# Kernel tuning notes

Hardware: AMD Instinct MI355X
Metric: run time of the kernel (lower is better)

The kernel has to match this reference:

```python
import jax, jax.numpy as jnp
import numpy as np

N, M, D = 8192, 8192, 1024

def setup_inputs() -> dict:
    key = jax.random.key(0)
    k1, k2 = jax.random.split(key)
    encoder_outputs = jax.random.normal(k1, (N, D), dtype=jnp.float32)
    fact_emb = jax.random.normal(k2, (M, D), dtype=jnp.float32)
    return {"encoder_outputs": encoder_outputs, "fact_emb": fact_emb}

def reference(encoder_outputs, fact_emb):
    # energy: [N, M] = encoder_outputs @ fact_emb^T (unscaled)
    energy = jnp.einsum('nd,md->nm', encoder_outputs, fact_emb)
    weights = jax.nn.softmax(energy, axis=1)          # softmax over facts
    outputs = jnp.einsum('nm,md->nd', weights, fact_emb)
    return (outputs, weights)
```

## Files before the change

kernel.cpp:

```cpp
#include <hip/hip_runtime.h>
#include <hip/hip_bf16.h>
#include <math.h>
#include <stdint.h>

#define N_ROWS 8192
#define M_FACTS 8192
#define D_DIM 1024

typedef __bf16 bf16x8_t __attribute__((ext_vector_type(8)));
typedef __bf16 bf16x4_t __attribute__((ext_vector_type(4)));
typedef float f32x4_t __attribute__((ext_vector_type(4)));

#define BM 128
#define BN 128
#define BK 32
#define PADK 40

__device__ __forceinline__ void gload_lds16(const void* g, void* lds) {
  __builtin_amdgcn_global_load_lds(
      (__attribute__((address_space(1))) void*)(uintptr_t)g,
      (__attribute__((address_space(3))) void*)(uint32_t)(uintptr_t)lds,
      16, 0, 0);
}


__global__ __launch_bounds__(256) void split_hi_lo(const float* __restrict__ X,
                                                   __bf16* __restrict__ H,
                                                   __bf16* __restrict__ L) {
  int i = blockIdx.x * 256 + threadIdx.x;
  float4 v = ((const float4*)X)[i];
  float f[4] = {v.x, v.y, v.z, v.w};
  bf16x4_t h, l;
#pragma unroll
  for (int q = 0; q < 4; q++) {
    __bf16 hh = (__bf16)f[q];
    h[q] = hh;
    l[q] = (__bf16)(f[q] - (float)hh);
  }
  ((bf16x4_t*)H)[i] = h;
  ((bf16x4_t*)L)[i] = l;
}

__global__ __launch_bounds__(256) void split_concat_E(const float* __restrict__ X,
                                                      __bf16* __restrict__ A2) {
  int idx = blockIdx.x * 256 + threadIdx.x;
  int n = idx >> 8, d4 = idx & 255;
  float4 v = ((const float4*)X)[idx];
  float f[4] = {v.x, v.y, v.z, v.w};
  bf16x4_t h, l;
#pragma unroll
  for (int q = 0; q < 4; q++) {
    __bf16 hh = (__bf16)f[q];
    h[q] = hh;
    l[q] = (__bf16)(f[q] - (float)hh);
  }
  size_t base = (size_t)n * 3072 + d4 * 4;
  *(bf16x4_t*)(A2 + base) = h;
  *(bf16x4_t*)(A2 + base + 1024) = l;
  *(bf16x4_t*)(A2 + base + 2048) = h;
}

__global__ __launch_bounds__(256) void split_concat_F(const float* __restrict__ X,
                                                      __bf16* __restrict__ B2) {
  int idx = blockIdx.x * 256 + threadIdx.x;
  int m = idx >> 8, d4 = idx & 255;
  float4 v = ((const float4*)X)[idx];
  float f[4] = {v.x, v.y, v.z, v.w};
  bf16x4_t h, l;
#pragma unroll
  for (int q = 0; q < 4; q++) {
    __bf16 hh = (__bf16)f[q];
    h[q] = hh;
    l[q] = (__bf16)(f[q] - (float)hh);
  }
  size_t base = (size_t)m * 3072 + d4 * 4;
  *(bf16x4_t*)(B2 + base) = h;
  *(bf16x4_t*)(B2 + base + 1024) = h;
  *(bf16x4_t*)(B2 + base + 2048) = l;
}

__global__ __launch_bounds__(256) void transpose_f_bf16(const float* __restrict__ F,
                                                        __bf16* __restrict__ Ft) {
  __shared__ float t[64 * 69];
  const int tid = threadIdx.x;
  const int m0 = blockIdx.x * 64, d0 = blockIdx.y * 64;
#pragma unroll
  for (int p = 0; p < 4; p++) {
    int flat = p * 256 + tid;
    int m = flat >> 4, dq = flat & 15;
    float4 v = *(const float4*)(F + (size_t)(m0 + m) * D_DIM + d0 + dq * 4);
    t[(dq * 4 + 0) * 69 + m] = v.x;
    t[(dq * 4 + 1) * 69 + m] = v.y;
    t[(dq * 4 + 2) * 69 + m] = v.z;
    t[(dq * 4 + 3) * 69 + m] = v.w;
  }
  __syncthreads();
#pragma unroll
  for (int q = 0; q < 2; q++) {
    int id = q * 256 + tid;
    int d = id >> 3, c = id & 7;
    const float* row = t + d * 69 + c * 8;
    bf16x8_t o;
#pragma unroll
    for (int i = 0; i < 8; i++) o[i] = (__bf16)row[i];
    *(bf16x8_t*)(Ft + (size_t)(d0 + d) * M_FACTS + m0 + c * 8) = o;
  }
}

__global__ __launch_bounds__(512, 2) void gemm_ring(const __bf16* __restrict__ A,
                                                    const __bf16* __restrict__ B,
                                                    float* __restrict__ C,
                                                    int K, int lda, int ldb, int ldc) {
  __shared__ __align__(16) __bf16 sA[3][256 * 64];
  __shared__ __align__(16) __bf16 sB[3][128 * 64];
  const int tid = threadIdx.x;
  const int wave = tid >> 6, lane = tid & 63;
  const int wm = wave >> 2;
  const int wn = wave & 3;
  const int lrow = lane & 15, quad = lane >> 4;
  const int row0 = blockIdx.x * 256;
  const int col0 = blockIdx.y * 128;

  auto STAGE = [&](int slot, int kt) {
    const int ko = kt * 64;
#pragma unroll
    for (int k = 0; k < 4; k++) {
      int g = tid + 512 * k;
      int sr = g >> 3;
      int so = ((g & 7) ^ (sr & 7)) << 3;
      gload_lds16(A + (size_t)(row0 + sr) * lda + ko + so, &sA[slot][g * 8]);
    }
#pragma unroll
    for (int k = 0; k < 2; k++) {
      int g = tid + 512 * k;
      int sr = g >> 3;
      int so = ((g & 7) ^ (sr & 7)) << 3;
      gload_lds16(B + (size_t)(col0 + sr) * ldb + ko + so, &sB[slot][g * 8]);
    }
  };

  f32x4_t acc[8][2];
#pragma unroll
  for (int i = 0; i < 8; i++)
#pragma unroll
    for (int j = 0; j < 2; j++) acc[i][j] = (f32x4_t){0.f, 0.f, 0.f, 0.f};

  const int nkt = K >> 6;

  STAGE(0, 0);
  STAGE(1, 1);
  asm volatile("s_waitcnt vmcnt(6)" ::: "memory");
  __builtin_amdgcn_s_barrier();
  __builtin_amdgcn_sched_barrier(0);

  int slot = 0;
  for (int t = 0; t < nkt; ++t) {
    const __bf16* lA = &sA[slot][0];
    const __bf16* lB = &sB[slot][0];
    const int slot2 = (slot == 0) ? 2 : slot - 1;

#pragma unroll
    for (int p = 0; p < 2; ++p) {
      bf16x8_t af[4][2], bfr[2][2];
#pragma unroll
      for (int rf = 0; rf < 4; ++rf) {
        const int r = wm * 128 + p * 64 + rf * 16 + lrow;
#pragma unroll
        for (int ks = 0; ks < 2; ++ks)
          af[rf][ks] = *(const bf16x8_t*)(lA + r * 64 + (((ks * 4 + quad) ^ (r & 7)) << 3));
      }
#pragma unroll
      for (int cf = 0; cf < 2; ++cf) {
        const int c = wn * 32 + cf * 16 + lrow;
#pragma unroll
        for (int ks = 0; ks < 2; ++ks)
          bfr[cf][ks] = *(const bf16x8_t*)(lB + c * 64 + (((ks * 4 + quad) ^ (c & 7)) << 3));
      }
      if (p == 0 && t + 2 < nkt) STAGE(slot2, t + 2);
      __builtin_amdgcn_s_setprio(1);
#pragma unroll
      for (int rf = 0; rf < 4; ++rf)
#pragma unroll
        for (int cf = 0; cf < 2; ++cf)
#pragma unroll
          for (int ks = 0; ks < 2; ++ks)
            acc[p * 4 + rf][cf] = __builtin_amdgcn_mfma_f32_16x16x32_bf16(
                af[rf][ks], bfr[cf][ks], acc[p * 4 + rf][cf], 0, 0, 0);
      __builtin_amdgcn_s_setprio(0);
      if (p == 0) {
        __builtin_amdgcn_sched_barrier(0);
        __builtin_amdgcn_s_barrier();
        __builtin_amdgcn_sched_barrier(0);
      }
    }
    __builtin_amdgcn_sched_barrier(0);
    if (t + 1 < nkt) {
      if (t + 2 < nkt)
        asm volatile("s_waitcnt vmcnt(6)" ::: "memory");
      else
        asm volatile("s_waitcnt vmcnt(0)" ::: "memory");
      __builtin_amdgcn_s_barrier();
      __builtin_amdgcn_sched_barrier(0);
    }
    slot = (slot == 2) ? 0 : slot + 1;
  }

#pragma unroll
  for (int i = 0; i < 8; ++i) {
    const int rbase = row0 + wm * 128 + (i >> 2) * 64 + (i & 3) * 16 + quad * 4;
#pragma unroll
    for (int j = 0; j < 2; ++j) {
      const int c = col0 + wn * 32 + j * 16 + lrow;
#pragma unroll
      for (int r = 0; r < 4; ++r) C[(size_t)(rbase + r) * ldc + c] = acc[i][j][r];
    }
  }
}

__global__ __launch_bounds__(256) void gemm1_fast(const __bf16* __restrict__ Eh,
                                                  const __bf16* __restrict__ El,
                                                  const __bf16* __restrict__ Fh,
                                                  const __bf16* __restrict__ Fl,
                                                  float* __restrict__ C,
                                                  int row_base) {
  __shared__ __bf16 sAh[BM * BK], sAl[BM * BK], sBh[BN * BK], sBl[BN * BK];
  const int tid = threadIdx.x;
  const int wave = tid >> 6, lane = tid & 63;
  const int row0 = row_base + blockIdx.x * BM, col0 = blockIdx.y * BN;
  const int wm = wave >> 1, wn = wave & 1;
  const int lrow = lane & 15, quad = lane >> 4;

  f32x4_t acc[4][4];
#pragma unroll
  for (int i = 0; i < 4; i++)
#pragma unroll
    for (int j = 0; j < 4; j++) acc[i][j] = (f32x4_t){0.f, 0.f, 0.f, 0.f};

  for (int k0 = 0; k0 < D_DIM; k0 += BK) {
#pragma unroll
    for (int r = 0; r < 2; r++) {
      int c = (r * 4 + wave) * 64 + lane;
      int row = c >> 2;
      int ko = (c & 3) << 3;
      size_t ga = (size_t)(row0 + row) * D_DIM + k0 + ko;
      size_t gb = (size_t)(col0 + row) * D_DIM + k0 + ko;
      gload_lds16(Eh + ga, sAh + c * 8);
      gload_lds16(El + ga, sAl + c * 8);
      gload_lds16(Fh + gb, sBh + c * 8);
      gload_lds16(Fl + gb, sBl + c * 8);
    }
    __syncthreads();

    bf16x8_t ah[4], al[4], bh[4], bl[4];
#pragma unroll
    for (int i = 0; i < 4; i++) {
      int ra = (wm * 64 + i * 16 + lrow) * BK + quad * 8;
      ah[i] = *(const bf16x8_t*)(sAh + ra);
      al[i] = *(const bf16x8_t*)(sAl + ra);
      int rb = (wn * 64 + i * 16 + lrow) * BK + quad * 8;
      bh[i] = *(const bf16x8_t*)(sBh + rb);
      bl[i] = *(const bf16x8_t*)(sBl + rb);
    }
#pragma unroll
    for (int i = 0; i < 4; i++)
#pragma unroll
      for (int j = 0; j < 4; j++) {
        acc[i][j] = __builtin_amdgcn_mfma_f32_16x16x32_bf16(ah[i], bh[j], acc[i][j], 0, 0, 0);
        acc[i][j] = __builtin_amdgcn_mfma_f32_16x16x32_bf16(ah[i], bl[j], acc[i][j], 0, 0, 0);
        acc[i][j] = __builtin_amdgcn_mfma_f32_16x16x32_bf16(al[i], bh[j], acc[i][j], 0, 0, 0);
      }
    __syncthreads();
  }

#pragma unroll
  for (int i = 0; i < 4; i++) {
    int rbase = row0 + wm * 64 + i * 16 + quad * 4;
#pragma unroll
    for (int j = 0; j < 4; j++) {
      int c = col0 + wn * 64 + j * 16 + lrow;
#pragma unroll
      for (int r = 0; r < 4; r++) C[(size_t)(rbase + r) * M_FACTS + c] = acc[i][j][r];
    }
  }
}

__global__ __launch_bounds__(256) void gemm2_reg(const __bf16* __restrict__ Wb,
                                                 const __bf16* __restrict__ Ft,
                                                 float* __restrict__ O,
                                                 int out_row0) {
  __shared__ __bf16 sW[2][BM * BK];
  __shared__ __bf16 sF[2][BN * BK];
  const int tid = threadIdx.x;
  const int wave = tid >> 6, lane = tid & 63;
  const int row0 = blockIdx.x * BM;
  const int col0 = blockIdx.y * BN;
  const int wm = wave >> 1, wn = wave & 1;
  const int lrow = lane & 15, quad = lane >> 4;

  const int id0 = wave * 64 + lane;
  const int r0 = id0 >> 2, c0 = (id0 & 3) << 3;
  const int id1 = id0 + 256;
  const int r1 = id1 >> 2, c1 = (id1 & 3) << 3;

  const __bf16* gW = Wb + (size_t)row0 * M_FACTS;
  const __bf16* gF = Ft + (size_t)col0 * M_FACTS;

  f32x4_t acc[4][4];
#pragma unroll
  for (int i = 0; i < 4; i++)
#pragma unroll
    for (int j = 0; j < 4; j++) acc[i][j] = (f32x4_t){0.f, 0.f, 0.f, 0.f};

  bf16x8_t rW0, rW1, rF0, rF1;
  rW0 = *(const bf16x8_t*)(gW + (size_t)r0 * M_FACTS + c0);
  rW1 = *(const bf16x8_t*)(gW + (size_t)r1 * M_FACTS + c1);
  rF0 = *(const bf16x8_t*)(gF + (size_t)r0 * M_FACTS + c0);
  rF1 = *(const bf16x8_t*)(gF + (size_t)r1 * M_FACTS + c1);
  *(bf16x8_t*)(&sW[0][id0 * 8]) = rW0;
  *(bf16x8_t*)(&sW[0][id1 * 8]) = rW1;
  *(bf16x8_t*)(&sF[0][id0 * 8]) = rF0;
  *(bf16x8_t*)(&sF[0][id1 * 8]) = rF1;
  rW0 = *(const bf16x8_t*)(gW + (size_t)r0 * M_FACTS + BK + c0);
  rW1 = *(const bf16x8_t*)(gW + (size_t)r1 * M_FACTS + BK + c1);
  rF0 = *(const bf16x8_t*)(gF + (size_t)r0 * M_FACTS + BK + c0);
  rF1 = *(const bf16x8_t*)(gF + (size_t)r1 * M_FACTS + BK + c1);
  __syncthreads();

  const int NT = M_FACTS / BK;
  for (int it = 0; it < NT; it++) {
    const int cur = it & 1;
    bf16x8_t a[4], b[4];
#pragma unroll
    for (int i = 0; i < 4; i++) {
      a[i] = *(const bf16x8_t*)(&sW[cur][(wm * 64 + i * 16 + lrow) * BK + quad * 8]);
      b[i] = *(const bf16x8_t*)(&sF[cur][(wn * 64 + i * 16 + lrow) * BK + quad * 8]);
    }
#pragma unroll
    for (int i = 0; i < 4; i++)
#pragma unroll
      for (int j = 0; j < 4; j++)
        acc[i][j] = __builtin_amdgcn_mfma_f32_16x16x32_bf16(a[i], b[j], acc[i][j], 0, 0, 0);

    __syncthreads();
    if (it + 1 < NT) {
      const int nxt = cur ^ 1;
      *(bf16x8_t*)(&sW[nxt][id0 * 8]) = rW0;
      *(bf16x8_t*)(&sW[nxt][id1 * 8]) = rW1;
      *(bf16x8_t*)(&sF[nxt][id0 * 8]) = rF0;
      *(bf16x8_t*)(&sF[nxt][id1 * 8]) = rF1;
      if (it + 2 < NT) {
        const int ko = (it + 2) * BK;
        rW0 = *(const bf16x8_t*)(gW + (size_t)r0 * M_FACTS + ko + c0);
        rW1 = *(const bf16x8_t*)(gW + (size_t)r1 * M_FACTS + ko + c1);
        rF0 = *(const bf16x8_t*)(gF + (size_t)r0 * M_FACTS + ko + c0);
        rF1 = *(const bf16x8_t*)(gF + (size_t)r1 * M_FACTS + ko + c1);
      }
      __syncthreads();
    }
  }

#pragma unroll
  for (int i = 0; i < 4; i++) {
    int rbase = out_row0 + row0 + wm * 64 + i * 16 + quad * 4;
#pragma unroll
    for (int j = 0; j < 4; j++) {
      int c = col0 + wn * 64 + j * 16 + lrow;
#pragma unroll
      for (int r = 0; r < 4; r++) O[(size_t)(rbase + r) * D_DIM + c] = acc[i][j][r];
    }
  }
}

__global__ __launch_bounds__(256) void gemm2_mid(const float* __restrict__ W,
                                                 const __bf16* __restrict__ Ft,
                                                 float* __restrict__ O) {
  __shared__ __bf16 sW[BM * BK], sF[BN * BK];
  const int tid = threadIdx.x;
  const int wave = tid >> 6, lane = tid & 63;
  const int row0 = blockIdx.x * BM, col0 = blockIdx.y * BN;
  const int wm = wave >> 1, wn = wave & 1;
  const int lrow = lane & 15, quad = lane >> 4;

  f32x4_t acc[4][4];
#pragma unroll
  for (int i = 0; i < 4; i++)
#pragma unroll
    for (int j = 0; j < 4; j++) acc[i][j] = (f32x4_t){0.f, 0.f, 0.f, 0.f};

  for (int k0 = 0; k0 < M_FACTS; k0 += BK) {
#pragma unroll
    for (int r = 0; r < 2; r++) {
      int c = (r * 4 + wave) * 64 + lane;
      int row = c >> 2;
      int ko = (c & 3) << 3;
      gload_lds16(Ft + (size_t)(col0 + row) * M_FACTS + k0 + ko, sF + c * 8);
    }
#pragma unroll
    for (int it = 0; it < 4; it++) {
      int flat = it * 256 + tid;
      int r = flat >> 3, q = flat & 7;
      float4 v = *(const float4*)(W + (size_t)(row0 + r) * M_FACTS + k0 + q * 4);
      bf16x4_t h;
      h[0] = (__bf16)v.x;
      h[1] = (__bf16)v.y;
      h[2] = (__bf16)v.z;
      h[3] = (__bf16)v.w;
      *(bf16x4_t*)(sW + r * BK + q * 4) = h;
    }
    __syncthreads();

    bf16x8_t a[4], b[4];
#pragma unroll
    for (int i = 0; i < 4; i++) {
      a[i] = *(const bf16x8_t*)(sW + (wm * 64 + i * 16 + lrow) * BK + quad * 8);
      b[i] = *(const bf16x8_t*)(sF + (wn * 64 + i * 16 + lrow) * BK + quad * 8);
    }
#pragma unroll
    for (int i = 0; i < 4; i++)
#pragma unroll
      for (int j = 0; j < 4; j++)
        acc[i][j] = __builtin_amdgcn_mfma_f32_16x16x32_bf16(a[i], b[j], acc[i][j], 0, 0, 0);
    __syncthreads();
  }

#pragma unroll
  for (int i = 0; i < 4; i++) {
    int rbase = row0 + wm * 64 + i * 16 + quad * 4;
#pragma unroll
    for (int j = 0; j < 4; j++) {
      int c = col0 + wn * 64 + j * 16 + lrow;
#pragma unroll
      for (int r = 0; r < 4; r++) O[(size_t)(rbase + r) * D_DIM + c] = acc[i][j][r];
    }
  }
}

template <bool EMIT_BF16>
__global__ __launch_bounds__(256) void softmax_rows_t(float* __restrict__ W,
                                                      __bf16* __restrict__ Wb) {
  __shared__ float red[8];
  const int tid = threadIdx.x;
  float* p = W + (size_t)blockIdx.x * M_FACTS;

  float4 v[8];
  float mx = -3.4e38f;
#pragma unroll
  for (int i = 0; i < 8; i++) {
    v[i] = *(const float4*)(p + (size_t)(i * 256 + tid) * 4);
    mx = fmaxf(mx, fmaxf(fmaxf(v[i].x, v[i].y), fmaxf(v[i].z, v[i].w)));
  }
#pragma unroll
  for (int off = 32; off >= 1; off >>= 1) mx = fmaxf(mx, __shfl_xor(mx, off));
  const int wave = tid >> 6, lane = tid & 63;
  if (lane == 0) red[wave] = mx;
  __syncthreads();
  mx = fmaxf(fmaxf(red[0], red[1]), fmaxf(red[2], red[3]));

  float s = 0.f;
#pragma unroll
  for (int i = 0; i < 8; i++) {
    v[i].x = __expf(v[i].x - mx);
    v[i].y = __expf(v[i].y - mx);
    v[i].z = __expf(v[i].z - mx);
    v[i].w = __expf(v[i].w - mx);
    s += v[i].x + v[i].y + v[i].z + v[i].w;
  }
#pragma unroll
  for (int off = 32; off >= 1; off >>= 1) s += __shfl_xor(s, off);
  if (lane == 0) red[4 + wave] = s;
  __syncthreads();
  s = red[4] + red[5] + red[6] + red[7];
  float inv = 1.0f / s;
  __bf16* pb = EMIT_BF16 ? (Wb + (size_t)blockIdx.x * M_FACTS) : nullptr;
#pragma unroll
  for (int i = 0; i < 8; i++) {
    v[i].x *= inv;
    v[i].y *= inv;
    v[i].z *= inv;
    v[i].w *= inv;
    *(float4*)(p + (size_t)(i * 256 + tid) * 4) = v[i];
    if (EMIT_BF16) {
      bf16x4_t h;
      h[0] = (__bf16)v[i].x;
      h[1] = (__bf16)v[i].y;
      h[2] = (__bf16)v[i].z;
      h[3] = (__bf16)v[i].w;
      *(bf16x4_t*)(pb + (size_t)(i * 256 + tid) * 4) = h;
    }
  }
}

__global__ __launch_bounds__(256) void gemm1_energy(const float* __restrict__ A,
                                                    const float* __restrict__ B,
                                                    float* __restrict__ C) {
  __shared__ __align__(16) __bf16 sAh[BM * PADK];
  __shared__ __align__(16) __bf16 sAl[BM * PADK];
  __shared__ __align__(16) __bf16 sBh[BN * PADK];
  __shared__ __align__(16) __bf16 sBl[BN * PADK];

  const int tid = threadIdx.x;
  const int row0 = blockIdx.x * BM, col0 = blockIdx.y * BN;
  const int wave = tid >> 6, lane = tid & 63;
  const int wm = wave >> 1, wn = wave & 1;
  const int lrow = lane & 15, quad = lane >> 4;

  f32x4_t acc[4][4];
#pragma unroll
  for (int i = 0; i < 4; i++)
#pragma unroll
    for (int j = 0; j < 4; j++) acc[i][j] = (f32x4_t){0.f, 0.f, 0.f, 0.f};

  for (int k0 = 0; k0 < D_DIM; k0 += BK) {
    __syncthreads();
#pragma unroll
    for (int it = 0; it < 4; it++) {
      int flat = it * 256 + tid;
      int r = flat >> 3, kq = flat & 7;
      float4 va = *(const float4*)(A + (size_t)(row0 + r) * D_DIM + k0 + kq * 4);
      float4 vb = *(const float4*)(B + (size_t)(col0 + r) * D_DIM + k0 + kq * 4);
      float fa[4] = {va.x, va.y, va.z, va.w};
      float fb[4] = {vb.x, vb.y, vb.z, vb.w};
      bf16x4_t ah, al, bh, bl;
#pragma unroll
      for (int q = 0; q < 4; q++) {
        __bf16 h = (__bf16)fa[q];
        ah[q] = h;
        al[q] = (__bf16)(fa[q] - (float)h);
        __bf16 g = (__bf16)fb[q];
        bh[q] = g;
        bl[q] = (__bf16)(fb[q] - (float)g);
      }
      *(bf16x4_t*)(sAh + r * PADK + kq * 4) = ah;
      *(bf16x4_t*)(sAl + r * PADK + kq * 4) = al;
      *(bf16x4_t*)(sBh + r * PADK + kq * 4) = bh;
      *(bf16x4_t*)(sBl + r * PADK + kq * 4) = bl;
    }
    __syncthreads();

    bf16x8_t a_h[4], a_l[4], b_h[4], b_l[4];
#pragma unroll
    for (int i = 0; i < 4; i++) {
      int ra = wm * 64 + i * 16 + lrow;
      a_h[i] = *(const bf16x8_t*)(sAh + ra * PADK + quad * 8);
      a_l[i] = *(const bf16x8_t*)(sAl + ra * PADK + quad * 8);
      int rb = wn * 64 + i * 16 + lrow;
      b_h[i] = *(const bf16x8_t*)(sBh + rb * PADK + quad * 8);
      b_l[i] = *(const bf16x8_t*)(sBl + rb * PADK + quad * 8);
    }
#pragma unroll
    for (int i = 0; i < 4; i++)
#pragma unroll
      for (int j = 0; j < 4; j++) {
        acc[i][j] = __builtin_amdgcn_mfma_f32_16x16x32_bf16(a_h[i], b_h[j], acc[i][j], 0, 0, 0);
        acc[i][j] = __builtin_amdgcn_mfma_f32_16x16x32_bf16(a_h[i], b_l[j], acc[i][j], 0, 0, 0);
        acc[i][j] = __builtin_amdgcn_mfma_f32_16x16x32_bf16(a_l[i], b_h[j], acc[i][j], 0, 0, 0);
      }
  }

#pragma unroll
  for (int i = 0; i < 4; i++) {
    int rbase = row0 + wm * 64 + i * 16 + quad * 4;
#pragma unroll
    for (int j = 0; j < 4; j++) {
      int c = col0 + wn * 64 + j * 16 + lrow;
#pragma unroll
      for (int r = 0; r < 4; r++) C[(size_t)(rbase + r) * M_FACTS + c] = acc[i][j][r];
    }
  }
}

__global__ __launch_bounds__(256) void gemm2_out(const float* __restrict__ W,
                                                 const float* __restrict__ F,
                                                 float* __restrict__ O) {
  __shared__ __align__(16) __bf16 sW[BM * PADK];
  __shared__ __align__(16) __bf16 sFt[BN * PADK];

  const int tid = threadIdx.x;
  const int row0 = blockIdx.x * BM, col0 = blockIdx.y * BN;
  const int wave = tid >> 6, lane = tid & 63;
  const int wm = wave >> 1, wn = wave & 1;
  const int lrow = lane & 15, quad = lane >> 4;

  f32x4_t acc[4][4];
#pragma unroll
  for (int i = 0; i < 4; i++)
#pragma unroll
    for (int j = 0; j < 4; j++) acc[i][j] = (f32x4_t){0.f, 0.f, 0.f, 0.f};

  for (int k0 = 0; k0 < M_FACTS; k0 += BK) {
    __syncthreads();
#pragma unroll
    for (int it = 0; it < 4; it++) {
      int flat = it * 256 + tid;
      int r = flat >> 3, kq = flat & 7;
      float4 v = *(const float4*)(W + (size_t)(row0 + r) * M_FACTS + k0 + kq * 4);
      bf16x4_t h;
      h[0] = (__bf16)v.x;
      h[1] = (__bf16)v.y;
      h[2] = (__bf16)v.z;
      h[3] = (__bf16)v.w;
      *(bf16x4_t*)(sW + r * PADK + kq * 4) = h;
    }
#pragma unroll
    for (int it = 0; it < 4; it++) {
      int flat = it * 256 + tid;
      int m = flat >> 5, dq = flat & 31;
      float4 v = *(const float4*)(F + (size_t)(k0 + m) * D_DIM + col0 + dq * 4);
      sFt[(dq * 4 + 0) * PADK + m] = (__bf16)v.x;
      sFt[(dq * 4 + 1) * PADK + m] = (__bf16)v.y;
      sFt[(dq * 4 + 2) * PADK + m] = (__bf16)v.z;
      sFt[(dq * 4 + 3) * PADK + m] = (__bf16)v.w;
    }
    __syncthreads();

    bf16x8_t a[4], b[4];
#pragma unroll
    for (int i = 0; i < 4; i++) {
      a[i] = *(const bf16x8_t*)(sW + (wm * 64 + i * 16 + lrow) * PADK + quad * 8);
      b[i] = *(const bf16x8_t*)(sFt + (wn * 64 + i * 16 + lrow) * PADK + quad * 8);
    }
#pragma unroll
    for (int i = 0; i < 4; i++)
#pragma unroll
      for (int j = 0; j < 4; j++)
        acc[i][j] = __builtin_amdgcn_mfma_f32_16x16x32_bf16(a[i], b[j], acc[i][j], 0, 0, 0);
  }

#pragma unroll
  for (int i = 0; i < 4; i++) {
    int rbase = row0 + wm * 64 + i * 16 + quad * 4;
#pragma unroll
    for (int j = 0; j < 4; j++) {
      int c = col0 + wn * 64 + j * 16 + lrow;
#pragma unroll
      for (int r = 0; r < 4; r++) O[(size_t)(rbase + r) * D_DIM + c] = acc[i][j][r];
    }
  }
}

extern "C" void kernel_launch(void* const* d_in, const int* in_sizes, int n_in,
                              void* d_out, int out_size, void* d_ws, size_t ws_size,
                              hipStream_t stream) {
  const float* E = (const float*)d_in[0];
  const float* F = (const float*)d_in[1];
  float* outputs = (float*)d_out;
  float* weights = (float*)d_out + (size_t)N_ROWS * D_DIM;

  const size_t MB = 1ull << 20;
  char* ws = (char*)d_ws;

  const bool t1 = ws_size >= 144 * MB;
  const bool t2 = !t1 && ws_size >= 80 * MB;
  const bool hasFtOnly = !t1 && !t2 && ws_size >= 16 * MB;

  if (t1) {
    __bf16* Ft = (__bf16*)(ws + 0 * MB);
    __bf16* A2 = (__bf16*)(ws + 16 * MB);
    __bf16* B2 = (__bf16*)(ws + 64 * MB);
    __bf16* Wb = (__bf16*)(ws + 16 * MB);

    transpose_f_bf16<<<dim3(M_FACTS / 64, D_DIM / 64), 256, 0, stream>>>(F, Ft);
    split_concat_E<<<dim3((N_ROWS * D_DIM) / 1024), 256, 0, stream>>>(E, A2);
    split_concat_F<<<dim3((M_FACTS * D_DIM) / 1024), 256, 0, stream>>>(F, B2);

    gemm_ring<<<dim3(N_ROWS / 256, M_FACTS / 128), 512, 0, stream>>>(
        A2, B2, weights, 3072, 3072, 3072, M_FACTS);

    softmax_rows_t<true><<<dim3(N_ROWS), 256, 0, stream>>>(weights, Wb);

    gemm_ring<<<dim3(N_ROWS / 256, D_DIM / 128), 512, 0, stream>>>(
        Wb, Ft, outputs, M_FACTS, M_FACTS, M_FACTS, D_DIM);
  } else if (t2) {
    __bf16* Ft = (__bf16*)(ws + 0 * MB);
    __bf16* Eh = (__bf16*)(ws + 16 * MB);
    __bf16* El = (__bf16*)(ws + 32 * MB);
    __bf16* Fh = (__bf16*)(ws + 48 * MB);
    __bf16* Fl = (__bf16*)(ws + 64 * MB);
    __bf16* Wb = (__bf16*)(ws + 16 * MB);

    transpose_f_bf16<<<dim3(M_FACTS / 64, D_DIM / 64), 256, 0, stream>>>(F, Ft);
    split_hi_lo<<<dim3((N_ROWS * D_DIM) / 1024), 256, 0, stream>>>(E, Eh, El);
    split_hi_lo<<<dim3((M_FACTS * D_DIM) / 1024), 256, 0, stream>>>(F, Fh, Fl);
    gemm1_fast<<<dim3(N_ROWS / BM, M_FACTS / BN), 256, 0, stream>>>(Eh, El, Fh, Fl,
                                                                    weights, 0);
    const int HALF = N_ROWS / 2;
    for (int h = 0; h < 2; h++) {
      float* Wchunk = weights + (size_t)h * HALF * M_FACTS;
      softmax_rows_t<true><<<dim3(HALF), 256, 0, stream>>>(Wchunk, Wb);
      gemm2_reg<<<dim3(HALF / BM, D_DIM / BN), 256, 0, stream>>>(Wb, Ft, outputs, h * HALF);
    }
  } else {
    __bf16* Ft = (__bf16*)ws;
    if (hasFtOnly) {
      transpose_f_bf16<<<dim3(M_FACTS / 64, D_DIM / 64), 256, 0, stream>>>(F, Ft);
    }
    gemm1_energy<<<dim3(N_ROWS / BM, M_FACTS / BN), 256, 0, stream>>>(E, F, weights);
    softmax_rows_t<false><<<dim3(N_ROWS), 256, 0, stream>>>(weights, nullptr);
    if (hasFtOnly) {
      gemm2_mid<<<dim3(N_ROWS / BM, D_DIM / BN), 256, 0, stream>>>(weights, Ft, outputs);
    } else {
      gemm2_out<<<dim3(N_ROWS / BM, D_DIM / BN), 256, 0, stream>>>(weights, F, outputs);
    }
  }
}
```

Baseline: 963.1 us.

## Replace triple-buffered GEMM ring with templated 256-wide-tile double-buffered GEMM

Replaces the 256x128 triple-buffered gemm_ring with a templated gemm_big that uses 256-column tiles (256x256 for the energy GEMM, 128x256 for the output GEMM). The pipeline becomes double-buffered with a single barrier per K-step and a full vmcnt(0) wait. Larger tiles raise arithmetic intensity and cut global/LDS traffic per MFMA. In exchange, each thread holds more accumulator registers, prefetch overlap is shallower, and the second GEMM launches fewer blocks (64x4).

New measurement: 944.5 us. No clear change (-1.9%).

```diff
diff --git a/kernel.cpp b/kernel.cpp
--- a/kernel.cpp
+++ b/kernel.cpp
@@ -107,110 +107,105 @@
   }
 }
 
-__global__ __launch_bounds__(512, 2) void gemm_ring(const __bf16* __restrict__ A,
-                                                    const __bf16* __restrict__ B,
-                                                    float* __restrict__ C,
-                                                    int K, int lda, int ldb, int ldc) {
-  __shared__ __align__(16) __bf16 sA[3][256 * 64];
-  __shared__ __align__(16) __bf16 sB[3][128 * 64];
+template <int RH>
+__global__ __launch_bounds__(512, 2) void gemm_big(const __bf16* __restrict__ A,
+                                                   const __bf16* __restrict__ B,
+                                                   float* __restrict__ C,
+                                                   int K, int lda, int ldb, int ldc) {
+  constexpr int BMT = RH * 128;
+  __shared__ __align__(16) __bf16 sA[2][BMT * 64];
+  __shared__ __align__(16) __bf16 sB[2][256 * 64];
   const int tid = threadIdx.x;
   const int wave = tid >> 6, lane = tid & 63;
   const int wm = wave >> 2;
   const int wn = wave & 3;
   const int lrow = lane & 15, quad = lane >> 4;
-  const int row0 = blockIdx.x * 256;
-  const int col0 = blockIdx.y * 128;
-
-  auto STAGE = [&](int slot, int kt) {
+  const int row0 = blockIdx.x * BMT;
+  const int col0 = blockIdx.y * 256;
+
+  auto STAGE = [&](int buf, int kt) {
     const int ko = kt * 64;
+#pragma unroll
+    for (int k = 0; k < RH * 2; k++) {
+      int g = tid + 512 * k;
+      int sr = g >> 3;
+      int so = ((g & 7) ^ (sr & 7)) << 3;
+      gload_lds16(A + (size_t)(row0 + sr) * lda + ko + so, &sA[buf][g * 8]);
+    }
 #pragma unroll
     for (int k = 0; k < 4; k++) {
       int g = tid + 512 * k;
       int sr = g >> 3;
       int so = ((g & 7) ^ (sr & 7)) << 3;
-      gload_lds16(A + (size_t)(row0 + sr) * lda + ko + so, &sA[slot][g * 8]);
-    }
-#pragma unroll
-    for (int k = 0; k < 2; k++) {
-      int g = tid + 512 * k;
-      int sr = g >> 3;
-      int so = ((g & 7) ^ (sr & 7)) << 3;
-      gload_lds16(B + (size_t)(col0 + sr) * ldb + ko + so, &sB[slot][g * 8]);
+      gload_lds16(B + (size_t)(col0 + sr) * ldb + ko + so, &sB[buf][g * 8]);
     }
   };
 
-  f32x4_t acc[8][2];
-#pragma unroll
-  for (int i = 0; i < 8; i++)
-#pragma unroll
-    for (int j = 0; j < 2; j++) acc[i][j] = (f32x4_t){0.f, 0.f, 0.f, 0.f};
+  f32x4_t acc[RH * 4][4];
+#pragma unroll
+  for (int i = 0; i < RH * 4; i++)
+#pragma unroll
+    for (int j = 0; j < 4; j++) acc[i][j] = (f32x4_t){0.f, 0.f, 0.f, 0.f};
 
   const int nkt = K >> 6;
 
   STAGE(0, 0);
-  STAGE(1, 1);
-  asm volatile("s_waitcnt vmcnt(6)" ::: "memory");
+  asm volatile("s_waitcnt vmcnt(0)" ::: "memory");
   __builtin_amdgcn_s_barrier();
   __builtin_amdgcn_sched_barrier(0);
 
-  int slot = 0;
   for (int t = 0; t < nkt; ++t) {
-    const __bf16* lA = &sA[slot][0];
-    const __bf16* lB = &sB[slot][0];
-    const int slot2 = (slot == 0) ? 2 : slot - 1;
-
-#pragma unroll
-    for (int p = 0; p < 2; ++p) {
-      bf16x8_t af[4][2], bfr[2][2];
+    const int cur = t & 1;
+    const __bf16* lA = &sA[cur][0];
+    const __bf16* lB = &sB[cur][0];
+
+    if (t + 1 < nkt) STAGE(cur ^ 1, t + 1);
+    __builtin_amdgcn_sched_barrier(0);
+
+    bf16x8_t bfr[4][2];
+#pragma unroll
+    for (int cf = 0; cf < 4; ++cf) {
+      const int c = wn * 64 + cf * 16 + lrow;
+#pragma unroll
+      for (int ks = 0; ks < 2; ++ks)
+        bfr[cf][ks] = *(const bf16x8_t*)(lB + c * 64 + (((ks * 4 + quad) ^ (c & 7)) << 3));
+    }
+#pragma unroll
+    for (int rh = 0; rh < RH; ++rh) {
+      bf16x8_t af[4][2];
 #pragma unroll
       for (int rf = 0; rf < 4; ++rf) {
-        const int r = wm * 128 + p * 64 + rf * 16 + lrow;
+        const int r = wm * (RH * 64) + rh * 64 + rf * 16 + lrow;
 #pragma unroll
         for (int ks = 0; ks < 2; ++ks)
           af[rf][ks] = *(const bf16x8_t*)(lA + r * 64 + (((ks * 4 + quad) ^ (r & 7)) << 3));
       }
-#pragma unroll
-      for (int cf = 0; cf < 2; ++cf) {
-        const int c = wn * 32 + cf * 16 + lrow;
-#pragma unroll
-        for (int ks = 0; ks < 2; ++ks)
-          bfr[cf][ks] = *(const bf16x8_t*)(lB + c * 64 + (((ks * 4 + quad) ^ (c & 7)) << 3));
-      }
-      if (p == 0 && t + 2 < nkt) STAGE(slot2, t + 2);
       __builtin_amdgcn_s_setprio(1);
 #pragma unroll
       for (int rf = 0; rf < 4; ++rf)
 #pragma unroll
-        for (int cf = 0; cf < 2; ++cf)
+        for (int cf = 0; cf < 4; ++cf)
 #pragma unroll
           for (int ks = 0; ks < 2; ++ks)
-            acc[p * 4 + rf][cf] = __builtin_amdgcn_mfma_f32_16x16x32_bf16(
-                af[rf][ks], bfr[cf][ks], acc[p * 4 + rf][cf], 0, 0, 0);
+            acc[rh * 4 + rf][cf] = __builtin_amdgcn_mfma_f32_16x16x32_bf16(
+                af[rf][ks], bfr[cf][ks], acc[rh * 4 + rf][cf], 0, 0, 0);
       __builtin_amdgcn_s_setprio(0);
-      if (p == 0) {
-        __builtin_amdgcn_sched_barrier(0);
-        __builtin_amdgcn_s_barrier();
-        __builtin_amdgcn_sched_barrier(0);
-      }
-    }
+    }
+
     __builtin_amdgcn_sched_barrier(0);
     if (t + 1 < nkt) {
-      if (t + 2 < nkt)
-        asm volatile("s_waitcnt vmcnt(6)" ::: "memory");
-      else
-        asm volatile("s_waitcnt vmcnt(0)" ::: "memory");
+      asm volatile("s_waitcnt vmcnt(0)" ::: "memory");
       __builtin_amdgcn_s_barrier();
       __builtin_amdgcn_sched_barrier(0);
     }
-    slot = (slot == 2) ? 0 : slot + 1;
-  }
-
-#pragma unroll
-  for (int i = 0; i < 8; ++i) {
-    const int rbase = row0 + wm * 128 + (i >> 2) * 64 + (i & 3) * 16 + quad * 4;
-#pragma unroll
-    for (int j = 0; j < 2; ++j) {
-      const int c = col0 + wn * 32 + j * 16 + lrow;
+  }
+
+#pragma unroll
+  for (int i = 0; i < RH * 4; ++i) {
+    const int rbase = row0 + wm * (RH * 64) + (i >> 2) * 64 + (i & 3) * 16 + quad * 4;
+#pragma unroll
+    for (int j = 0; j < 4; ++j) {
+      const int c = col0 + wn * 64 + j * 16 + lrow;
 #pragma unroll
       for (int r = 0; r < 4; ++r) C[(size_t)(rbase + r) * ldc + c] = acc[i][j][r];
     }
@@ -663,12 +658,12 @@
     split_concat_E<<<dim3((N_ROWS * D_DIM) / 1024), 256, 0, stream>>>(E, A2);
     split_concat_F<<<dim3((M_FACTS * D_DIM) / 1024), 256, 0, stream>>>(F, B2);
 
-    gemm_ring<<<dim3(N_ROWS / 256, M_FACTS / 128), 512, 0, stream>>>(
+    gemm_big<2><<<dim3(N_ROWS / 256, M_FACTS / 256), 512, 0, stream>>>(
         A2, B2, weights, 3072, 3072, 3072, M_FACTS);
 
     softmax_rows_t<true><<<dim3(N_ROWS), 256, 0, stream>>>(weights, Wb);
 
-    gemm_ring<<<dim3(N_ROWS / 256, D_DIM / 128), 512, 0, stream>>>(
+    gemm_big<1><<<dim3(N_ROWS / 128, D_DIM / 256), 512, 0, stream>>>(
         Wb, Ft, outputs, M_FACTS, M_FACTS, M_FACTS, D_DIM);
   } else if (t2) {
     __bf16* Ft = (__bf16*)(ws + 0 * MB);
```
